# Kernel optimization log

Hardware: AMD Instinct MI355X
Metric: run time of the kernel (lower is better)

## Reference

```python
import jax, jax.numpy as jnp
import numpy as np

B, T, F, H = 64, 1024, 160, 1024


def setup_inputs() -> dict:
    key = jax.random.key(0)
    ks = jax.random.split(key, 18)
    s = lambda k, shape, scale=0.05: (jax.random.normal(k, shape, jnp.float32) * scale)
    inp = {
        "x": jax.random.normal(ks[0], (B, T, F), jnp.float32),
        # encoder GRU layer 0 (input F -> hidden H), PyTorch gate order r,z,n
        "Wih0": s(ks[1], (3 * H, F)), "Whh0": s(ks[2], (3 * H, H)),
        "bih0": s(ks[3], (3 * H,)), "bhh0": s(ks[4], (3 * H,)),
        # encoder GRU layer 1 (input H -> hidden H)
        "Wih1": s(ks[5], (3 * H, H)), "Whh1": s(ks[6], (3 * H, H)),
        "bih1": s(ks[7], (3 * H,)), "bhh1": s(ks[8], (3 * H,)),
        # fc: (n_enc_layers*H) -> H
        "fcW": s(ks[9], (H, 2 * H)), "fcb": jnp.zeros((H,), jnp.float32),
        # decoder GRUCell (input F -> hidden H)
        "dWih": s(ks[10], (3 * H, F)), "dWhh": s(ks[11], (3 * H, H)),
        "dbih": s(ks[12], (3 * H,)), "dbhh": s(ks[13], (3 * H,)),
        # dec_proj: H -> F
        "pW": s(ks[14], (F, H)), "pb": jnp.zeros((F,), jnp.float32),
    }
    return inp


def gru_step(h, xt, Wih, Whh, bih, bhh):
    # PyTorch GRU/GRUCell math, gate order (r, z, n)
    gi = xt @ Wih.T + bih          # [B, 3H]
    gh = h @ Whh.T + bhh           # [B, 3H]
    ir, iz, inn = jnp.split(gi, 3, axis=-1)
    hr, hz, hn = jnp.split(gh, 3, axis=-1)
    r = jax.nn.sigmoid(ir + hr)
    z = jax.nn.sigmoid(iz + hz)
    n = jnp.tanh(inn + r * hn)
    return (1.0 - z) * n + z * h


def reference(x, Wih0, Whh0, bih0, bhh0, Wih1, Whh1, bih1, bhh1,
              fcW, fcb, dWih, dWhh, dbih, dbhh, pW, pb):
    Bx, Tx = x.shape[0], x.shape[1]
    xs = jnp.swapaxes(x, 0, 1)  # [T, B, F]

    def run_layer(seq, Wih, Whh, bih, bhh):
        h0 = jnp.zeros((Bx, Whh.shape[1]), x.dtype)
        def step(h, xt):
            h = gru_step(h, xt, Wih, Whh, bih, bhh)
            return h, h
        hT, hs = jax.lax.scan(step, h0, seq)
        return hT, hs

    # 2-layer encoder GRU (dropout disabled: eval-mode / deterministic reference)
    h1, hs0 = run_layer(xs, Wih0, Whh0, bih0, bhh0)
    h2, _ = run_layer(hs0, Wih1, Whh1, bih1, bhh1)

    # h_n permute+view -> concat(layer0, layer1) along features
    h = jnp.tanh(jnp.concatenate([h1, h2], axis=-1) @ fcW.T + fcb)  # [B, H]

    i0 = jnp.zeros((Bx, pW.shape[0]), x.dtype)
    def dec_step(carry, _):
        hd, i = carry
        hd = gru_step(hd, i, dWih, dWhh, dbih, dbhh)
        i = hd @ pW.T + pb
        return (hd, i), i
    _, outs = jax.lax.scan(dec_step, (h, i0), None, length=Tx)  # [T, B, F]
    return jnp.swapaxes(outs, 0, 1)  # [B, T, F]
```

## Files before the change

### kernel.cpp

```cpp
#include <hip/hip_runtime.h>
#include <math.h>

#define NWG 256
#define NTH 512

typedef _Float16 f16;
typedef __attribute__((ext_vector_type(8))) _Float16 h8;
typedef __attribute__((ext_vector_type(4))) float f4;

namespace {
constexpr int T_ = 1024, F_ = 160, H_ = 1024;
constexpr float SC = 2048.f;
constexpr float INV = 1.f / 2048.f;

constexpr int ESLOTH = 512 * 64 * 8;
constexpr int DSLOTH = 256 * 64 * 8;
constexpr int ELO = 256;
constexpr int DLO = 128;

constexpr size_t WS_BAR  = 0;
constexpr size_t WS_CVEC = 2048;
constexpr size_t WS_WDEC = 14336;
constexpr size_t WS_ENCA = WS_WDEC + (size_t)4 * H_ * H_ * 4;
constexpr size_t WS_DECA = WS_ENCA + (size_t)2 * ESLOTH * 2;
constexpr size_t WS_STRM = WS_DECA + (size_t)2 * DSLOTH * 2;

constexpr int DBUF_B = 135168;
constexpr int TBUF_B = DBUF_B + 17408;
constexpr int ZP_B   = TBUF_B + 2048;
constexpr int LDS_B  = ZP_B + 64;
}

__device__ __forceinline__ f4 MF(h8 a, h8 b, f4 c) {
  return __builtin_amdgcn_mfma_f32_16x16x32_f16(a, b, c, 0, 0, 0);
}

__device__ __forceinline__ void fsplit(float v, f16& hi, f16& lo) {
  const float hf = (fabsf(v) >= 6.103515625e-05f) ? (float)(f16)v : 0.f;
  hi = (f16)hf;
  lo = (f16)((v - hf) * SC);
}

__device__ __forceinline__ void gbar(unsigned* bar, int wg, unsigned& phase) {
  __syncthreads();
  ++phase;
  if (threadIdx.x == 0) {
    unsigned* grp = bar + ((wg >> 5) << 5);
    unsigned old = __hip_atomic_fetch_add(grp, 1u, __ATOMIC_ACQ_REL, __HIP_MEMORY_SCOPE_AGENT);
    if ((old & 31u) == 31u) {
      unsigned r = __hip_atomic_fetch_add(bar + 256, 1u, __ATOMIC_ACQ_REL, __HIP_MEMORY_SCOPE_AGENT);
      if ((r & 7u) == 7u)
        __hip_atomic_fetch_add(bar + 288, 1u, __ATOMIC_ACQ_REL, __HIP_MEMORY_SCOPE_AGENT);
    }
    while (__hip_atomic_load(bar + 288, __ATOMIC_RELAXED, __HIP_MEMORY_SCOPE_AGENT) < phase)
      __builtin_amdgcn_s_sleep(1);
    (void)__hip_atomic_load(bar + 288, __ATOMIC_ACQUIRE, __HIP_MEMORY_SCOPE_AGENT);
  }
  __syncthreads();
}

__device__ void stageEnc(f16* __restrict__ whi, f16* __restrict__ wlo,
                         const float* __restrict__ Wx, const float* __restrict__ Wh,
                         int KX, int XOo, int KO, int u0, int tid) {
  for (int task = tid; task < KO * 24; task += NTH) {
    const int oct = task / 24;
    const int sl = task - oct * 24;
    const int g = (sl < 16) ? (sl >> 3) : 2;
    const int u = u0 + (sl & 7);
    const float* src = (oct < XOo)
        ? (Wx + (size_t)(g * H_ + u) * KX + (size_t)oct * 8)
        : (Wh + (size_t)(g * H_ + u) * H_ + (size_t)(oct - XOo) * 8);
    const float4 a = *(const float4*)src;
    const float4 b = *(const float4*)(src + 4);
    const float v[8] = {a.x, a.y, a.z, a.w, b.x, b.y, b.z, b.w};
    h8 hv, lv;
#pragma unroll
    for (int e = 0; e < 8; ++e) { f16 hh, ll; fsplit(v[e], hh, ll); hv[e] = hh; lv[e] = ll; }
    *(h8*)(whi + ((size_t)oct * 25 + sl) * 8) = hv;
    if (wlo) *(h8*)(wlo + ((size_t)oct * 25 + sl) * 8) = lv;
  }
}

__device__ void stageDec(f16* __restrict__ whi, f16* __restrict__ wlo,
                         const float* __restrict__ wdec, const float* __restrict__ dWhh,
                         int u0, int tid, bool t1set) {
  for (int task = tid; task < 128 * 32; task += NTH) {
    const int oct = task >> 5, sl = task & 31;
    const int g = sl >> 3;
    const int u = u0 + (sl & 7);
    float v[8];
    if (t1set) {
      if (g == 2) {
#pragma unroll
        for (int e = 0; e < 8; ++e) v[e] = 0.f;
      } else {
        const float* s = dWhh + (size_t)((g == 3 ? 2 : g) * H_ + u) * H_ + (size_t)oct * 8;
        const float4 a = *(const float4*)s, b = *(const float4*)(s + 4);
        v[0]=a.x; v[1]=a.y; v[2]=a.z; v[3]=a.w; v[4]=b.x; v[5]=b.y; v[6]=b.z; v[7]=b.w;
      }
    } else {
      const float* s = wdec + (size_t)(g * H_ + u) * H_ + (size_t)oct * 8;
      const float4 a = *(const float4*)s, b = *(const float4*)(s + 4);
      v[0]=a.x; v[1]=a.y; v[2]=a.z; v[3]=a.w; v[4]=b.x; v[5]=b.y; v[6]=b.z; v[7]=b.w;
    }
    h8 hv, lv;
#pragma unroll
    for (int e = 0; e < 8; ++e) { f16 hh, ll; fsplit(v[e], hh, ll); hv[e] = hh; lv[e] = ll; }
    *(h8*)(whi + ((size_t)oct * 33 + sl) * 8) = hv;
    *(h8*)(wlo + ((size_t)oct * 33 + sl) * 8) = lv;
  }
}

__device__ void stageProj(f16* __restrict__ whi, f16* __restrict__ wlo,
                          const float* __restrict__ pW, int f0, int tid) {
  for (int task = tid; task < 128 * 16; task += NTH) {
    const int oct = task >> 4, sl = task & 15;
    const float* s = pW + (size_t)(f0 + sl) * H_ + (size_t)oct * 8;
    const float4 a = *(const float4*)s, b = *(const float4*)(s + 4);
    const float v[8] = {a.x, a.y, a.z, a.w, b.x, b.y, b.z, b.w};
    h8 hv, lv;
#pragma unroll
    for (int e = 0; e < 8; ++e) { f16 hh, ll; fsplit(v[e], hh, ll); hv[e] = hh; lv[e] = ll; }
    *(h8*)(whi + ((size_t)oct * 17 + sl) * 8) = hv;
    *(h8*)(wlo + ((size_t)oct * 17 + sl) * 8) = lv;
  }
}

template<int NT, bool NSPLIT, int ROWH, bool STRM>
__device__ __forceinline__ void gmm(f4* Dh, f4* Dc,
    const f16* __restrict__ Ab, int aoctBase, int loOct,
    const f16* __restrict__ whi, const f16* __restrict__ wlo,
    const f16* __restrict__ strm,
    int ktn, int octBase, int XO, int ls, int lq, int lane,
    const f16* __restrict__ zp) {
  auto LD = [&](int kk, h8& ah, h8& al, h8& bh0, h8& bl0, h8& bh1, h8& bl1) {
    const int aoct = aoctBase + kk * 4 + lq;
    ah = *(const h8*)(Ab + (size_t)aoct * 512);
    al = *(const h8*)(Ab + (size_t)(aoct + loOct) * 512);
    const int oct = octBase + kk * 4 + lq;
    bh0 = *(const h8*)(whi + ((size_t)oct * ROWH + ls) * 8);
    if constexpr (STRM) bl0 = *(const h8*)(strm + ((size_t)(kk * 2) * 64 + lane) * 8);
    else bl0 = *(const h8*)(wlo + ((size_t)oct * ROWH + ls) * 8);
    if constexpr (NT == 2) {
      bool act = true; int psl;
      if constexpr (NSPLIT) { act = (ls < 8) ? (oct < XO) : (oct >= XO); psl = 16 + (ls & 7); }
      else { psl = 16 + ls; }
      bh1 = *(const h8*)(act ? (whi + ((size_t)oct * ROWH + psl) * 8) : zp);
      if constexpr (STRM) bl1 = *(const h8*)(strm + ((size_t)(kk * 2 + 1) * 64 + lane) * 8);
      else bl1 = *(const h8*)(act ? (wlo + ((size_t)oct * ROWH + psl) * 8) : zp);
    }
  };
  h8 ah, al, bh0, bl0, bh1, bl1;
  LD(0, ah, al, bh0, bl0, bh1, bl1);
  for (int kk = 0; kk < ktn; ++kk) {
    h8 ah2, al2, bh02, bl02, bh12, bl12;
    const int nk = (kk + 1 < ktn) ? (kk + 1) : kk;
    LD(nk, ah2, al2, bh02, bl02, bh12, bl12);
    Dh[0] = MF(ah, bh0, Dh[0]);
    Dc[0] = MF(al, bh0, Dc[0]);
    Dc[0] = MF(ah, bl0, Dc[0]);
    if constexpr (NT == 2) {
      Dh[1] = MF(ah, bh1, Dh[1]);
      Dc[1] = MF(al, bh1, Dc[1]);
      Dc[1] = MF(ah, bl1, Dc[1]);
    }
    ah = ah2; al = al2; bh0 = bh02; bl0 = bl02;
    if constexpr (NT == 2) { bh1 = bh12; bl1 = bl12; }
  }
}

__device__ __forceinline__ void gmm_x(f4* Dh, f4* Dc, const float* __restrict__ xp,
    const f16* __restrict__ whi, const f16* __restrict__ wlo,
    int ls, int lq, const f16* __restrict__ zp) {
#pragma unroll
  for (int kk = 0; kk < 5; ++kk) {
    const float4 a = *(const float4*)(xp + kk * 32);
    const float4 b = *(const float4*)(xp + kk * 32 + 4);
    const float v[8] = {a.x, a.y, a.z, a.w, b.x, b.y, b.z, b.w};
    h8 ah, al;
#pragma unroll
    for (int e = 0; e < 8; ++e) { f16 hh, ll; fsplit(v[e], hh, ll); ah[e] = hh; al[e] = ll; }
    const int oct = kk * 4 + lq;
    {
      const h8 bh2 = *(const h8*)(whi + ((size_t)oct * 25 + ls) * 8);
      const h8 bl2 = *(const h8*)(wlo + ((size_t)oct * 25 + ls) * 8);
      Dh[0] = MF(ah, bh2, Dh[0]);
      Dc[0] = MF(al, bh2, Dc[0]);
      Dc[0] = MF(ah, bl2, Dc[0]);
    }
    {
      const bool act = (ls < 8);
      const int psl = 16 + (ls & 7);
      const h8 bh2 = *(const h8*)(act ? (whi + ((size_t)oct * 25 + psl) * 8) : zp);
      const h8 bl2 = *(const h8*)(act ? (wlo + ((size_t)oct * 25 + psl) * 8) : zp);
      Dh[1] = MF(ah, bh2, Dh[1]);
      Dc[1] = MF(al, bh2, Dc[1]);
      Dc[1] = MF(ah, bl2, Dc[1]);
    }
  }
}

__global__ void build_c_kernel(const float* __restrict__ dWih, const float* __restrict__ dbih,
                               const float* __restrict__ pb, float* __restrict__ cvec) {
  const int r = blockIdx.x * 256 + threadIdx.x;
  if (r >= 3 * H_) return;
  float a = dbih[r];
  for (int f = 0; f < F_; ++f) a += dWih[(size_t)r * F_ + f] * pb[f];
  cvec[r] = a;
}

__global__ void build_wdec_kernel(const float* __restrict__ dWih, const float* __restrict__ dWhh,
                                  const float* __restrict__ pW, float* __restrict__ wdec) {
  const int idx = blockIdx.x * 256 + threadIdx.x;
  if (idx >= 3 * H_ * 128) return;
  const int row = idx >> 7;
  const int oct = idx & 127;
  float v[8] = {0, 0, 0, 0, 0, 0, 0, 0};
  const float* wr = dWih + (size_t)row * F_;
  for (int f = 0; f < F_; ++f) {
    const float w = wr[f];
    const float4 p0 = *(const float4*)(pW + (size_t)f * H_ + oct * 8);
    const float4 p1 = *(const float4*)(pW + (size_t)f * H_ + oct * 8 + 4);
    v[0] += w * p0.x; v[1] += w * p0.y; v[2] += w * p0.z; v[3] += w * p0.w;
    v[4] += w * p1.x; v[5] += w * p1.y; v[6] += w * p1.z; v[7] += w * p1.w;
  }
  if ((row >> 10) < 2) {
    const float* hr = dWhh + (size_t)row * H_ + oct * 8;
#pragma unroll
    for (int e = 0; e < 8; ++e) v[e] += hr[e];
  }
  float* o = wdec + (size_t)row * H_ + oct * 8;
#pragma unroll
  for (int e = 0; e < 8; ++e) o[e] = v[e];
}
__global__ void build_wdec_nh(const float* __restrict__ dWhh, float* __restrict__ wdec) {
  const int idx = blockIdx.x * 256 + threadIdx.x;
  if (idx >= H_ * H_) return;
  wdec[(size_t)3 * H_ * H_ + idx] = dWhh[(size_t)2 * H_ * H_ + idx];
}

__global__ void build_strm(const float* __restrict__ Wih1, const float* __restrict__ Whh1,
                           f16* __restrict__ strm) {
  const size_t idx = (size_t)blockIdx.x * 256 + threadIdx.x;
  const int j = (int)(idx & 7);
  const int lane = (int)((idx >> 3) & 63);
  const int nt = (int)((idx >> 9) & 1);
  const int kk = (int)((idx >> 10) & 31);
  const int kb = (int)((idx >> 15) & 1);
  const int wg = (int)(idx >> 16);
  const int c = lane & 15, lq = lane >> 4;
  const int oct = kb * 128 + kk * 4 + lq;
  const int k = oct * 8 + j;
  float v = 0.f;
  if (nt == 0) {
    const int row = (c >> 3) * H_ + wg * 8 + (c & 7);
    v = (oct < 128) ? Wih1[(size_t)row * H_ + k] : Whh1[(size_t)row * H_ + (k - 1024)];
  } else {
    const bool act = (c < 8) ? (oct < 128) : (oct >= 128);
    if (act) {
      const int row = 2 * H_ + wg * 8 + (c & 7);
      v = (oct < 128) ? Wih1[(size_t)row * H_ + k] : Whh1[(size_t)row * H_ + (k - 1024)];
    }
  }
  f16 hh, ll; fsplit(v, hh, ll);
  strm[idx] = ll;
}

__global__ void __launch_bounds__(NTH, 1) speech_ae_persistent(
    const float* __restrict__ x,
    const float* __restrict__ Wih0, const float* __restrict__ Whh0,
    const float* __restrict__ bih0, const float* __restrict__ bhh0,
    const float* __restrict__ Wih1, const float* __restrict__ Whh1,
    const float* __restrict__ bih1, const float* __restrict__ bhh1,
    const float* __restrict__ fcW, const float* __restrict__ fcb,
    const float* __restrict__ dbih, const float* __restrict__ dbhh,
    const float* __restrict__ pW, const float* __restrict__ pb,
    const float* __restrict__ dWhh,
    float* __restrict__ out, void* ws) {
  extern __shared__ char ldsb[];
  f16* wh = (f16*)ldsb;
  float* dbuf = (float*)(ldsb + DBUF_B);
  float* tbuf = (float*)(ldsb + TBUF_B);
  f16* zp = (f16*)(ldsb + ZP_B);

  char* wsb = (char*)ws;
  unsigned* bar = (unsigned*)(wsb + WS_BAR);
  const float* cvec = (const float*)(wsb + WS_CVEC);
  const float* wdec = (const float*)(wsb + WS_WDEC);
  f16* encA = (f16*)(wsb + WS_ENCA);
  f16* decA = (f16*)(wsb + WS_DECA);
  const f16* strm = (const f16*)(wsb + WS_STRM);

  const int tid = threadIdx.x, wg = blockIdx.x;
  const int lane = tid & 63, wv = tid >> 6;
  const int ls = lane & 15, lq = lane >> 4;
  const int m0 = (wv & 3) * 16, kb = wv >> 2;
  const int mb = m0 + ls;
  const bool isL1 = (wg < 128);
  unsigned phase = 0;
  const f16* strmW = strm + (size_t)(wg * 2 + kb) * 32768;

  const float* bi = isL1 ? bih1 : bih0;
  const float* bh_ = isL1 ? bhh1 : bhh0;
  const int eru = (isL1 ? wg * 8 : (wg - 128) * 8) + wv;
  const float ebr = bi[eru] + bh_[eru];
  const float ebz = bi[H_ + eru] + bh_[H_ + eru];
  const float ebni = bi[2 * H_ + eru];
  const float ebnh = bh_[2 * H_ + eru];
  float hreg = 0.f;

  float b1r = 0, b1z = 0, b1ni = 0, b1nh = 0, bfr = 0, bfz = 0, bfni = 0, bfnh = 0, hdreg = 0.f;
  if (wg < 128) {
    const int rw = wg * 8 + wv;
    b1r = dbih[rw] + dbhh[rw];
    b1z = dbih[H_ + rw] + dbhh[H_ + rw];
    b1ni = dbih[2 * H_ + rw];
    b1nh = dbhh[2 * H_ + rw];
    bfr = cvec[rw] + dbhh[rw];
    bfz = cvec[H_ + rw] + dbhh[H_ + rw];
    bfni = cvec[2 * H_ + rw];
    bfnh = dbhh[2 * H_ + rw];
  }
  const int f0 = (wg - 128) * 16;
  float pbr[4] = {0, 0, 0, 0};
  if (wg >= 128 && wg < 138 && tid < 256) {
    const int fq = tid & 3;
#pragma unroll
    for (int e = 0; e < 4; ++e) pbr[e] = pb[f0 + fq * 4 + e];
  }

  if (isL1) stageEnc(wh, nullptr, Wih1, Whh1, H_, 128, 256, wg * 8, tid);
  else stageEnc(wh, wh + 29600, Wih0, Whh0, F_, 20, 148, (wg - 128) * 8, tid);
  if (tid < 16) zp[tid] = (f16)0.f;
  __syncthreads();

  for (int s = 0; s <= T_; ++s) {
    const bool active = isL1 ? (s >= 1) : (s < T_);
    if (active) {
      const int t = isL1 ? (s - 1) : s;
      f4 Dh[2] = {{0.f,0.f,0.f,0.f},{0.f,0.f,0.f,0.f}};
      f4 Dc[2] = {{0.f,0.f,0.f,0.f},{0.f,0.f,0.f,0.f}};
      if (isL1) {
        if (kb == 0) {
          const f16* Ab = encA + (size_t)(t & 1) * ESLOTH + (size_t)mb * 8;
          gmm<2, true, 25, true>(Dh, Dc, Ab, 0, ELO, wh, nullptr, strmW, 32, 0, 128, ls, lq, lane, zp);
        } else if (t >= 1) {
          const f16* Ab = encA + (size_t)((t - 1) & 1) * ESLOTH + (size_t)mb * 8;
          gmm<2, true, 25, true>(Dh, Dc, Ab, 128, ELO, wh, nullptr, strmW, 32, 128, 128, ls, lq, lane, zp);
        }
      } else {
        if (kb == 0) {
          const float* xp = x + ((size_t)mb * T_ + t) * F_ + lq * 8;
          gmm_x(Dh, Dc, xp, wh, wh + 29600, ls, lq, zp);
          if (t >= 1) {
            const f16* Ab = encA + (size_t)((t - 1) & 1) * ESLOTH + (size_t)mb * 8;
            gmm<2, true, 25, false>(Dh, Dc, Ab, 0, ELO, wh, wh + 29600, nullptr, 14, 20, 20, ls, lq, lane, zp);
          }
        } else if (t >= 1) {
          const f16* Ab = encA + (size_t)((t - 1) & 1) * ESLOTH + (size_t)mb * 8;
          gmm<2, true, 25, false>(Dh, Dc, Ab, 56, ELO, wh, wh + 29600, nullptr, 18, 76, 20, ls, lq, lane, zp);
        }
      }
      *(f4*)(dbuf + kb * 2176 + ls * 68 + m0 + lq * 4) = Dh[0] + Dc[0] * INV;
      *(f4*)(dbuf + kb * 2176 + (16 + ls) * 68 + m0 + lq * 4) = Dh[1] + Dc[1] * INV;
      __syncthreads();
      const int b = lane;
      const float gr  = dbuf[wv * 68 + b]        + dbuf[2176 + wv * 68 + b]        + ebr;
      const float gz  = dbuf[(8 + wv) * 68 + b]  + dbuf[2176 + (8 + wv) * 68 + b]  + ebz;
      const float gni = dbuf[(16 + wv) * 68 + b] + dbuf[2176 + (16 + wv) * 68 + b] + ebni;
      const float gnh = dbuf[(24 + wv) * 68 + b] + dbuf[2176 + (24 + wv) * 68 + b] + ebnh;
      const float rg = 1.f / (1.f + expf(-gr));
      const float zg = 1.f / (1.f + expf(-gz));
      const float ng = tanhf(gni + rg * gnh);
      const float hn = (1.f - zg) * ng + zg * hreg;
      hreg = hn;
      tbuf[wv * 64 + b] = hn;
      __syncthreads();
      if (tid < 64) {
        const int oct = isL1 ? (128 + wg) : (wg - 128);
        f16* dst = encA + (size_t)(t & 1) * ESLOTH + ((size_t)oct * 64 + tid) * 8;
        h8 hv, lv;
#pragma unroll
        for (int e = 0; e < 8; ++e) { f16 hh, ll; fsplit(tbuf[e * 64 + tid], hh, ll); hv[e] = hh; lv[e] = ll; }
        *(h8*)dst = hv;
        *(h8*)(dst + (size_t)ELO * 512) = lv;
      }
    }
    gbar(bar, wg, phase);
  }

  if (wg < 128) {
    const int u0f = wg * 8;
    const int b = lane;
    float acc[8] = {0, 0, 0, 0, 0, 0, 0, 0};
    for (int ko = wv * 32; ko < wv * 32 + 32; ++ko) {
      const f16* hp = encA + ESLOTH + ((size_t)ko * 64 + b) * 8;
      const h8 hiv = *(const h8*)hp;
      const h8 lov = *(const h8*)(hp + (size_t)ELO * 512);
      float hv[8];
#pragma unroll
      for (int e = 0; e < 8; ++e) hv[e] = (float)hiv[e] + (float)lov[e] * INV;
#pragma unroll
      for (int u = 0; u < 8; ++u) {
        const float* wr = fcW + (size_t)(u0f + u) * 2048 + (size_t)ko * 8;
        const float4 wa = *(const float4*)wr, wb = *(const float4*)(wr + 4);
        acc[u] += hv[0] * wa.x + hv[1] * wa.y + hv[2] * wa.z + hv[3] * wa.w
                + hv[4] * wb.x + hv[5] * wb.y + hv[6] * wb.z + hv[7] * wb.w;
      }
    }
    __syncthreads();
#pragma unroll
    for (int u = 0; u < 8; ++u) dbuf[(u * 8 + wv) * 68 + b] = acc[u];
    __syncthreads();
    float sum = fcb[u0f + wv];
#pragma unroll
    for (int g = 0; g < 8; ++g) sum += dbuf[(wv * 8 + g) * 68 + lane];
    tbuf[wv * 64 + lane] = tanhf(sum);
    __syncthreads();
    if (tid < 64) {
      f16* dst = decA + ((size_t)wg * 64 + tid) * 8;
      h8 hv, lv;
#pragma unroll
      for (int e = 0; e < 8; ++e) { f16 hh, ll; fsplit(tbuf[e * 64 + tid], hh, ll); hv[e] = hh; lv[e] = ll; }
      *(h8*)dst = hv;
      *(h8*)(dst + (size_t)DLO * 512) = lv;
    }
  }
  if (wg < 128) stageDec(wh, wh + 33792, nullptr, dWhh, wg * 8, tid, true);
  else if (wg < 138) stageProj(wh, wh + 17408, pW, f0, tid);
  gbar(bar, wg, phase);

  auto dec_step = [&](int t, bool first) {
    f4 Dh[2] = {{0.f,0.f,0.f,0.f},{0.f,0.f,0.f,0.f}};
    f4 Dc[2] = {{0.f,0.f,0.f,0.f},{0.f,0.f,0.f,0.f}};
    const f16* Ab = decA + (size_t)((t - 1) & 1) * DSLOTH + (size_t)mb * 8;
    gmm<2, false, 33, false>(Dh, Dc, Ab, kb * 64, DLO, wh, wh + 33792, nullptr, 16, kb * 64, 0, ls, lq, lane, zp);
    *(f4*)(dbuf + kb * 2176 + ls * 68 + m0 + lq * 4) = Dh[0] + Dc[0] * INV;
    *(f4*)(dbuf + kb * 2176 + (16 + ls) * 68 + m0 + lq * 4) = Dh[1] + Dc[1] * INV;
    __syncthreads();
    const int b = lane;
    float hprev;
    if (first) {
      const f16* r0 = decA + ((size_t)wg * 64 + b) * 8 + wv;
      hprev = (float)r0[0] + (float)r0[DLO * 512] * INV;
    } else hprev = hdreg;
    const float gr  = dbuf[wv * 68 + b]        + dbuf[2176 + wv * 68 + b]        + (first ? b1r : bfr);
    const float gz  = dbuf[(8 + wv) * 68 + b]  + dbuf[2176 + (8 + wv) * 68 + b]  + (first ? b1z : bfz);
    const float gni = dbuf[(16 + wv) * 68 + b] + dbuf[2176 + (16 + wv) * 68 + b] + (first ? b1ni : bfni);
    const float gnh = dbuf[(24 + wv) * 68 + b] + dbuf[2176 + (24 + wv) * 68 + b] + (first ? b1nh : bfnh);
    const float rg = 1.f / (1.f + expf(-gr));
    const float zg = 1.f / (1.f + expf(-gz));
    const float ng = tanhf(gni + rg * gnh);
    const float hn = (1.f - zg) * ng + zg * hprev;
    hdreg = hn;
    tbuf[wv * 64 + b] = hn;
    __syncthreads();
    if (tid < 64) {
      f16* dst = decA + (size_t)(t & 1) * DSLOTH + ((size_t)wg * 64 + tid) * 8;
      h8 hv, lv;
#pragma unroll
      for (int e = 0; e < 8; ++e) { f16 hh, ll; fsplit(tbuf[e * 64 + tid], hh, ll); hv[e] = hh; lv[e] = ll; }
      *(h8*)dst = hv;
      *(h8*)(dst + (size_t)DLO * 512) = lv;
    }
  };

  auto proj = [&](int t2) {
    f4 Dh[1] = {{0.f,0.f,0.f,0.f}};
    f4 Dc[1] = {{0.f,0.f,0.f,0.f}};
    const f16* Ab = decA + (size_t)((t2 - 1) & 1) * DSLOTH + (size_t)mb * 8;
    gmm<1, false, 17, false>(Dh, Dc, Ab, kb * 64, DLO, wh, wh + 17408, nullptr, 16, kb * 64, 0, ls, lq, lane, zp);
    *(f4*)(dbuf + kb * 2176 + ls * 68 + m0 + lq * 4) = Dh[0] + Dc[0] * INV;
    __syncthreads();
    if (tid < 256) {
      const int b2 = tid >> 2, fq = tid & 3;
      float4 o;
      o.x = dbuf[(fq * 4 + 0) * 68 + b2] + dbuf[2176 + (fq * 4 + 0) * 68 + b2] + pbr[0];
      o.y = dbuf[(fq * 4 + 1) * 68 + b2] + dbuf[2176 + (fq * 4 + 1) * 68 + b2] + pbr[1];
      o.z = dbuf[(fq * 4 + 2) * 68 + b2] + dbuf[2176 + (fq * 4 + 2) * 68 + b2] + pbr[2];
      o.w = dbuf[(fq * 4 + 3) * 68 + b2] + dbuf[2176 + (fq * 4 + 3) * 68 + b2] + pbr[3];
      *(float4*)(out + (size_t)b2 * (T_ * F_) + (size_t)(t2 - 2) * F_ + f0 + fq * 4) = o;
    }
  };

  if (wg < 128) dec_step(1, true);
  gbar(bar, wg, phase);
  if (wg < 128) {
    stageDec(wh, wh + 33792, wdec, nullptr, wg * 8, tid, false);
    __syncthreads();
  }

  for (int t2 = 2; t2 <= T_ + 1; ++t2) {
    if (wg < 128) {
      if (t2 <= T_) dec_step(t2, false);
    } else if (wg < 138) {
      proj(t2);
    }
    gbar(bar, wg, phase);
  }
}

extern "C" void kernel_launch(void* const* d_in, const int* in_sizes, int n_in,
                              void* d_out, int out_size, void* d_ws, size_t ws_size,
                              hipStream_t stream) {
  (void)in_sizes; (void)n_in; (void)out_size; (void)ws_size;
  const float* x    = (const float*)d_in[0];
  const float* Wih0 = (const float*)d_in[1];
  const float* Whh0 = (const float*)d_in[2];
  const float* bih0 = (const float*)d_in[3];
  const float* bhh0 = (const float*)d_in[4];
  const float* Wih1 = (const float*)d_in[5];
  const float* Whh1 = (const float*)d_in[6];
  const float* bih1 = (const float*)d_in[7];
  const float* bhh1 = (const float*)d_in[8];
  const float* fcW  = (const float*)d_in[9];
  const float* fcb  = (const float*)d_in[10];
  const float* dWih = (const float*)d_in[11];
  const float* dWhh = (const float*)d_in[12];
  const float* dbih = (const float*)d_in[13];
  const float* dbhh = (const float*)d_in[14];
  const float* pW   = (const float*)d_in[15];
  const float* pb   = (const float*)d_in[16];
  float* out = (float*)d_out;
  char* wsb = (char*)d_ws;

  hipFuncSetAttribute((const void*)speech_ae_persistent,
                      hipFuncAttributeMaxDynamicSharedMemorySize, LDS_B);
  hipMemsetAsync(d_ws, 0, 2048, stream);
  build_c_kernel<<<(3 * H_ + 255) / 256, 256, 0, stream>>>(dWih, dbih, pb, (float*)(wsb + WS_CVEC));
  build_wdec_kernel<<<(3 * H_ * 128 + 255) / 256, 256, 0, stream>>>(dWih, dWhh, pW, (float*)(wsb + WS_WDEC));
  build_wdec_nh<<<(H_ * H_ + 255) / 256, 256, 0, stream>>>(dWhh, (float*)(wsb + WS_WDEC));
  build_strm<<<32768, 256, 0, stream>>>(Wih1, Whh1, (f16*)(wsb + WS_STRM));
  speech_ae_persistent<<<NWG, NTH, LDS_B, stream>>>(
      x, Wih0, Whh0, bih0, bhh0, Wih1, Whh1, bih1, bhh1, fcW, fcb,
      dbih, dbhh, pW, pb, dWhh, out, d_ws);
}
```

Before: 38.83 ms.

## Use master-polled flag barrier, deeper global prefetch in gmm, and prefetch x inputs

Replaces the hierarchical atomic-counter grid barrier with a flag barrier: each workgroup stores its phase to its own slot, and one master workgroup polls all slots with a wavefront and then releases everyone. The gmm loop is templated on its trip count and fully unrolled, with a 4-deep register prefetch of the activation and streamed operands. The layer-0 input x for the next timestep is also loaded into registers before the barrier. Together these aim to cut the per-step barrier latency and the exposed global-load latency in the serial recurrence, at the cost of more registers and one serialised master workgroup.

```diff
diff --git a/kernel.cpp b/kernel.cpp
--- a/kernel.cpp
+++ b/kernel.cpp
@@ -3,6 +3,7 @@
 
 #define NWG 256
 #define NTH 512
+#define MASTER (NWG - 1)
 
 typedef _Float16 f16;
 typedef __attribute__((ext_vector_type(8))) _Float16 h8;
@@ -44,17 +45,31 @@
 __device__ __forceinline__ void gbar(unsigned* bar, int wg, unsigned& phase) {
   __syncthreads();
   ++phase;
-  if (threadIdx.x == 0) {
-    unsigned* grp = bar + ((wg >> 5) << 5);
-    unsigned old = __hip_atomic_fetch_add(grp, 1u, __ATOMIC_ACQ_REL, __HIP_MEMORY_SCOPE_AGENT);
-    if ((old & 31u) == 31u) {
-      unsigned r = __hip_atomic_fetch_add(bar + 256, 1u, __ATOMIC_ACQ_REL, __HIP_MEMORY_SCOPE_AGENT);
-      if ((r & 7u) == 7u)
-        __hip_atomic_fetch_add(bar + 288, 1u, __ATOMIC_ACQ_REL, __HIP_MEMORY_SCOPE_AGENT);
-    }
-    while (__hip_atomic_load(bar + 288, __ATOMIC_RELAXED, __HIP_MEMORY_SCOPE_AGENT) < phase)
-      __builtin_amdgcn_s_sleep(1);
-    (void)__hip_atomic_load(bar + 288, __ATOMIC_ACQUIRE, __HIP_MEMORY_SCOPE_AGENT);
+  const int tid = threadIdx.x;
+  if (wg == MASTER) {
+    if (tid < 64) {
+      if (tid == 0)
+        __hip_atomic_store(&bar[MASTER], phase, __ATOMIC_RELEASE, __HIP_MEMORY_SCOPE_AGENT);
+      for (;;) {
+        bool ok = true;
+#pragma unroll
+        for (int j = 0; j < 4; ++j)
+          ok &= (__hip_atomic_load(&bar[tid * 4 + j], __ATOMIC_RELAXED, __HIP_MEMORY_SCOPE_AGENT) >= phase);
+        if (__all(ok)) break;
+        __builtin_amdgcn_s_sleep(1);
+      }
+      if (tid == 0) {
+        __threadfence();
+        __hip_atomic_store(&bar[288], phase, __ATOMIC_RELEASE, __HIP_MEMORY_SCOPE_AGENT);
+      }
+    }
+  } else {
+    if (tid == 0) {
+      __hip_atomic_store(&bar[wg], phase, __ATOMIC_RELEASE, __HIP_MEMORY_SCOPE_AGENT);
+      while (__hip_atomic_load(&bar[288], __ATOMIC_RELAXED, __HIP_MEMORY_SCOPE_AGENT) < phase)
+        __builtin_amdgcn_s_sleep(1);
+      __threadfence();
+    }
   }
   __syncthreads();
 }
@@ -126,36 +141,45 @@
   }
 }
 
-template<int NT, bool NSPLIT, int ROWH, bool STRM>
+template<int KTN, int NT, bool NSPLIT, int ROWH, bool STRM>
 __device__ __forceinline__ void gmm(f4* Dh, f4* Dc,
     const f16* __restrict__ Ab, int aoctBase, int loOct,
     const f16* __restrict__ whi, const f16* __restrict__ wlo,
     const f16* __restrict__ strm,
-    int ktn, int octBase, int XO, int ls, int lq, int lane,
+    int octBase, int XO, int ls, int lq, int lane,
     const f16* __restrict__ zp) {
-  auto LD = [&](int kk, h8& ah, h8& al, h8& bh0, h8& bl0, h8& bh1, h8& bl1) {
+  constexpr int PF = (KTN < 4) ? KTN : 4;
+  h8 ahb[PF], alb[PF], bl0b[PF], bl1b[PF];
+  auto LDG = [&](int kk, h8& ah, h8& al, h8& bl0, h8& bl1) {
     const int aoct = aoctBase + kk * 4 + lq;
     ah = *(const h8*)(Ab + (size_t)aoct * 512);
     al = *(const h8*)(Ab + (size_t)(aoct + loOct) * 512);
+    if constexpr (STRM) {
+      bl0 = *(const h8*)(strm + ((size_t)(kk * 2) * 64 + lane) * 8);
+      if constexpr (NT == 2)
+        bl1 = *(const h8*)(strm + ((size_t)(kk * 2 + 1) * 64 + lane) * 8);
+    }
+  };
+#pragma unroll
+  for (int i = 0; i < PF; ++i) LDG(i, ahb[i], alb[i], bl0b[i], bl1b[i]);
+#pragma unroll
+  for (int kk = 0; kk < KTN; ++kk) {
+    const int sl = kk % PF;
     const int oct = octBase + kk * 4 + lq;
-    bh0 = *(const h8*)(whi + ((size_t)oct * ROWH + ls) * 8);
-    if constexpr (STRM) bl0 = *(const h8*)(strm + ((size_t)(kk * 2) * 64 + lane) * 8);
+    const h8 ah = ahb[sl], al = alb[sl];
+    const h8 bh0 = *(const h8*)(whi + ((size_t)oct * ROWH + ls) * 8);
+    h8 bl0, bh1, bl1;
+    if constexpr (STRM) bl0 = bl0b[sl];
     else bl0 = *(const h8*)(wlo + ((size_t)oct * ROWH + ls) * 8);
     if constexpr (NT == 2) {
       bool act = true; int psl;
       if constexpr (NSPLIT) { act = (ls < 8) ? (oct < XO) : (oct >= XO); psl = 16 + (ls & 7); }
       else { psl = 16 + ls; }
       bh1 = *(const h8*)(act ? (whi + ((size_t)oct * ROWH + psl) * 8) : zp);
-      if constexpr (STRM) bl1 = *(const h8*)(strm + ((size_t)(kk * 2 + 1) * 64 + lane) * 8);
+      if constexpr (STRM) bl1 = bl1b[sl];
       else bl1 = *(const h8*)(act ? (wlo + ((size_t)oct * ROWH + psl) * 8) : zp);
     }
-  };
-  h8 ah, al, bh0, bl0, bh1, bl1;
-  LD(0, ah, al, bh0, bl0, bh1, bl1);
-  for (int kk = 0; kk < ktn; ++kk) {
-    h8 ah2, al2, bh02, bl02, bh12, bl12;
-    const int nk = (kk + 1 < ktn) ? (kk + 1) : kk;
-    LD(nk, ah2, al2, bh02, bl02, bh12, bl12);
+    if (kk + PF < KTN) LDG(kk + PF, ahb[sl], alb[sl], bl0b[sl], bl1b[sl]);
     Dh[0] = MF(ah, bh0, Dh[0]);
     Dc[0] = MF(al, bh0, Dc[0]);
     Dc[0] = MF(ah, bl0, Dc[0]);
@@ -164,18 +188,16 @@
       Dc[1] = MF(al, bh1, Dc[1]);
       Dc[1] = MF(ah, bl1, Dc[1]);
     }
-    ah = ah2; al = al2; bh0 = bh02; bl0 = bl02;
-    if constexpr (NT == 2) { bh1 = bh12; bl1 = bl12; }
-  }
-}
-
-__device__ __forceinline__ void gmm_x(f4* Dh, f4* Dc, const float* __restrict__ xp,
+  }
+}
+
+__device__ __forceinline__ void gmm_x(f4* Dh, f4* Dc, const float4* __restrict__ xb,
     const f16* __restrict__ whi, const f16* __restrict__ wlo,
     int ls, int lq, const f16* __restrict__ zp) {
 #pragma unroll
   for (int kk = 0; kk < 5; ++kk) {
-    const float4 a = *(const float4*)(xp + kk * 32);
-    const float4 b = *(const float4*)(xp + kk * 32 + 4);
+    const float4 a = xb[kk * 2];
+    const float4 b = xb[kk * 2 + 1];
     const float v[8] = {a.x, a.y, a.z, a.w, b.x, b.y, b.z, b.w};
     h8 ah, al;
 #pragma unroll
@@ -334,6 +356,19 @@
   if (tid < 16) zp[tid] = (f16)0.f;
   __syncthreads();
 
+  float4 xb[10];
+  auto loadx = [&](int t) {
+    if (t < T_) {
+      const float* xp = x + ((size_t)mb * T_ + t) * F_ + lq * 8;
+#pragma unroll
+      for (int kk = 0; kk < 5; ++kk) {
+        xb[kk * 2]     = *(const float4*)(xp + kk * 32);
+        xb[kk * 2 + 1] = *(const float4*)(xp + kk * 32 + 4);
+      }
+    }
+  };
+  if (!isL1 && kb == 0) loadx(0);
+
   for (int s = 0; s <= T_; ++s) {
     const bool active = isL1 ? (s >= 1) : (s < T_);
     if (active) {
@@ -343,22 +378,21 @@
       if (isL1) {
         if (kb == 0) {
           const f16* Ab = encA + (size_t)(t & 1) * ESLOTH + (size_t)mb * 8;
-          gmm<2, true, 25, true>(Dh, Dc, Ab, 0, ELO, wh, nullptr, strmW, 32, 0, 128, ls, lq, lane, zp);
+          gmm<32, 2, true, 25, true>(Dh, Dc, Ab, 0, ELO, wh, nullptr, strmW, 0, 128, ls, lq, lane, zp);
         } else if (t >= 1) {
           const f16* Ab = encA + (size_t)((t - 1) & 1) * ESLOTH + (size_t)mb * 8;
-          gmm<2, true, 25, true>(Dh, Dc, Ab, 128, ELO, wh, nullptr, strmW, 32, 128, 128, ls, lq, lane, zp);
+          gmm<32, 2, true, 25, true>(Dh, Dc, Ab, 128, ELO, wh, nullptr, strmW, 128, 128, ls, lq, lane, zp);
         }
       } else {
         if (kb == 0) {
-          const float* xp = x + ((size_t)mb * T_ + t) * F_ + lq * 8;
-          gmm_x(Dh, Dc, xp, wh, wh + 29600, ls, lq, zp);
+          gmm_x(Dh, Dc, xb, wh, wh + 29600, ls, lq, zp);
           if (t >= 1) {
             const f16* Ab = encA + (size_t)((t - 1) & 1) * ESLOTH + (size_t)mb * 8;
-            gmm<2, true, 25, false>(Dh, Dc, Ab, 0, ELO, wh, wh + 29600, nullptr, 14, 20, 20, ls, lq, lane, zp);
+            gmm<14, 2, true, 25, false>(Dh, Dc, Ab, 0, ELO, wh, wh + 29600, nullptr, 20, 20, ls, lq, lane, zp);
           }
         } else if (t >= 1) {
           const f16* Ab = encA + (size_t)((t - 1) & 1) * ESLOTH + (size_t)mb * 8;
-          gmm<2, true, 25, false>(Dh, Dc, Ab, 56, ELO, wh, wh + 29600, nullptr, 18, 76, 20, ls, lq, lane, zp);
+          gmm<18, 2, true, 25, false>(Dh, Dc, Ab, 56, ELO, wh, wh + 29600, nullptr, 76, 20, ls, lq, lane, zp);
         }
       }
       *(f4*)(dbuf + kb * 2176 + ls * 68 + m0 + lq * 4) = Dh[0] + Dc[0] * INV;
@@ -385,6 +419,7 @@
         *(h8*)dst = hv;
         *(h8*)(dst + (size_t)ELO * 512) = lv;
       }
+      if (!isL1 && kb == 0) loadx(t + 1);
     }
     gbar(bar, wg, phase);
   }
@@ -434,7 +469,7 @@
     f4 Dh[2] = {{0.f,0.f,0.f,0.f},{0.f,0.f,0.f,0.f}};
     f4 Dc[2] = {{0.f,0.f,0.f,0.f},{0.f,0.f,0.f,0.f}};
     const f16* Ab = decA + (size_t)((t - 1) & 1) * DSLOTH + (size_t)mb * 8;
-    gmm<2, false, 33, false>(Dh, Dc, Ab, kb * 64, DLO, wh, wh + 33792, nullptr, 16, kb * 64, 0, ls, lq, lane, zp);
+    gmm<16, 2, false, 33, false>(Dh, Dc, Ab, kb * 64, DLO, wh, wh + 33792, nullptr, kb * 64, 0, ls, lq, lane, zp);
     *(f4*)(dbuf + kb * 2176 + ls * 68 + m0 + lq * 4) = Dh[0] + Dc[0] * INV;
     *(f4*)(dbuf + kb * 2176 + (16 + ls) * 68 + m0 + lq * 4) = Dh[1] + Dc[1] * INV;
     __syncthreads();
@@ -469,7 +504,7 @@
     f4 Dh[1] = {{0.f,0.f,0.f,0.f}};
     f4 Dc[1] = {{0.f,0.f,0.f,0.f}};
     const f16* Ab = decA + (size_t)((t2 - 1) & 1) * DSLOTH + (size_t)mb * 8;
-    gmm<1, false, 17, false>(Dh, Dc, Ab, kb * 64, DLO, wh, wh + 17408, nullptr, 16, kb * 64, 0, ls, lq, lane, zp);
+    gmm<16, 1, false, 17, false>(Dh, Dc, Ab, kb * 64, DLO, wh, wh + 17408, nullptr, kb * 64, 0, ls, lq, lane, zp);
     *(f4*)(dbuf + kb * 2176 + ls * 68 + m0 + lq * 4) = Dh[0] + Dc[0] * INV;
     __syncthreads();
     if (tid < 256) {
```

Result: slower. 77.66 ms (+100.0%).
